# Optimization experiments

Measured on AMD Instinct MI355X. Metric: run time of the kernel, lower is better.

The kernel has to match this reference:

```python
import jax, jax.numpy as jnp
import numpy as np

M, N, NS, E, FF, OUT, L = 65536, 200000, 32, 64, 128, 128, 2

def setup_inputs() -> dict:
    key = jax.random.key(0)
    ks = jax.random.split(key, 32)
    inp = {
        'xyz': jax.random.normal(ks[0], (N, 3), jnp.float32),
        'new_xyz': jax.random.normal(ks[1], (M, 3), jnp.float32),
        'features': jax.random.normal(ks[2], (N, E), jnp.float32),
        'group_idx': jax.random.randint(ks[3], (M, NS), 0, N, jnp.int32),
        'empty_mask': jnp.zeros((M,), jnp.bool_),
        # positional MLP: Conv2d(3->E//2,1x1,no bias) + BN + ReLU + Conv2d(E//2->E,1x1)
        'pos_w1': jax.random.normal(ks[4], (E // 2, 3), jnp.float32) * 0.5,
        'pos_bn_g': jnp.ones((E // 2,), jnp.float32),
        'pos_bn_b': jnp.zeros((E // 2,), jnp.float32),
        'pos_bn_mean': jnp.zeros((E // 2,), jnp.float32),
        'pos_bn_var': jnp.ones((E // 2,), jnp.float32),
        'pos_w2': jax.random.normal(ks[5], (E, E // 2), jnp.float32) * 0.2,
        'pos_b2': jnp.zeros((E,), jnp.float32),
        # 2 pre-norm transformer layers (stacked on leading dim)
        'ln1_g': jnp.ones((L, E), jnp.float32),
        'ln1_b': jnp.zeros((L, E), jnp.float32),
        'qkv_w': jax.random.normal(ks[6], (L, 3 * E, E), jnp.float32) * (E ** -0.5),
        'qkv_b': jnp.zeros((L, 3 * E), jnp.float32),
        'attn_out_w': jax.random.normal(ks[7], (L, E, E), jnp.float32) * (E ** -0.5),
        'attn_out_b': jnp.zeros((L, E), jnp.float32),
        'ln2_g': jnp.ones((L, E), jnp.float32),
        'ln2_b': jnp.zeros((L, E), jnp.float32),
        'ff1_w': jax.random.normal(ks[8], (L, FF, E), jnp.float32) * (E ** -0.5),
        'ff1_b': jnp.zeros((L, FF), jnp.float32),
        'ff2_w': jax.random.normal(ks[9], (L, E, FF), jnp.float32) * (FF ** -0.5),
        'ff2_b': jnp.zeros((L, E), jnp.float32),
        # output Conv1d(E->OUT,1)
        'out_w': jax.random.normal(ks[10], (OUT, E), jnp.float32) * (E ** -0.5),
        'out_b': jnp.zeros((OUT,), jnp.float32),
    }
    return inp


def _layernorm(v, g, b, eps=1e-5):
    mu = v.mean(-1, keepdims=True)
    var = v.var(-1, keepdims=True)
    return (v - mu) / jnp.sqrt(var + eps) * g + b


def reference(xyz, new_xyz, features, group_idx, empty_mask,
              pos_w1, pos_bn_g, pos_bn_b, pos_bn_mean, pos_bn_var, pos_w2, pos_b2,
              ln1_g, ln1_b, qkv_w, qkv_b, attn_out_w, attn_out_b,
              ln2_g, ln2_b, ff1_w, ff1_b, ff2_w, ff2_b, out_w, out_b):
    # neighbor gather (stand-in for VoxelQueryAndGrouping)
    gf = features[group_idx]                                  # (M, NS, E)
    gx = xyz[group_idx] - new_xyz[:, None, :]                  # (M, NS, 3) relative coords
    m = empty_mask[:, None, None]
    gf = jnp.where(m, 0.0, gf)
    gx = jnp.where(m, 0.0, gx)
    # positional encoding via 1x1 convs (= per-point linear) + BN (inference stats) + ReLU
    h = gx @ pos_w1.T
    h = (h - pos_bn_mean) * pos_bn_g / jnp.sqrt(pos_bn_var + 1e-5) + pos_bn_b
    pos = jax.nn.relu(h) @ pos_w2.T + pos_b2                   # (M, NS, E)
    x = gf + pos                                               # (B=M, L=NS, E)
    d = x.shape[-1]
    scale = 1.0 / jnp.sqrt(jnp.asarray(d, x.dtype))
    n_layers = qkv_w.shape[0]
    for l in range(n_layers):
        # pre-norm self-attention (nhead=1), dropout=0
        s = _layernorm(x, ln1_g[l], ln1_b[l])
        qkv = s @ qkv_w[l].T + qkv_b[l]                        # (M, NS, 3E)
        q, k, v = jnp.split(qkv, 3, axis=-1)
        attn = jax.nn.softmax(jnp.einsum('mie,mje->mij', q * scale, k), axis=-1)
        a = jnp.einsum('mij,mje->mie', attn, v) @ attn_out_w[l].T + attn_out_b[l]
        x = x + a
        # pre-norm FFN
        s = _layernorm(x, ln2_g[l], ln2_b[l])
        f = jax.nn.relu(s @ ff1_w[l].T + ff1_b[l]) @ ff2_w[l].T + ff2_b[l]
        x = x + f
    pooled = x.max(axis=1)                                     # max over nsample window
    return pooled @ out_w.T + out_b                            # (M, OUT)
```

## Files before the change

kernel.cpp:

```cpp
#include <hip/hip_runtime.h>
#include <hip/hip_bf16.h>
#include <math.h>

#define MQ   65536
#define OUTD 128
#define ARB  18944

typedef __attribute__((ext_vector_type(8))) short bf16x8;
typedef __attribute__((ext_vector_type(4))) short bf16x4;
typedef __attribute__((ext_vector_type(4))) float f32x4;

#define WS_QKV   0
#define WS_AOW   49152
#define WS_F1W   65536
#define WS_F2W   98304
#define WS_PW2   131072
#define WS_W1F   135168
#define WS_PBF   135552

__device__ __forceinline__ unsigned short f2bf(float f) {
  unsigned u = __float_as_uint(f);
  u = (u + 0x7FFFu + ((u >> 16) & 1u)) >> 16;
  return (unsigned short)u;
}

__device__ __forceinline__ f32x4 mfma16(bf16x8 a, bf16x8 b, f32x4 c) {
  return __builtin_amdgcn_mfma_f32_16x16x32_bf16(a, b, c, 0, 0, 0);
}

__device__ __forceinline__ unsigned pk2(float a, float b) {
  union { __hip_bfloat162 h; unsigned u; } c;
  float2 p; p.x = a; p.y = b;
  c.h = __float22bfloat162_rn(p);
  return c.u;
}

__device__ __forceinline__ bf16x4 pack4(f32x4 v) {
  union { unsigned u[2]; bf16x4 s; } c;
  c.u[0] = pk2(v[0], v[1]);
  c.u[1] = pk2(v[2], v[3]);
  return c.s;
}

__device__ __forceinline__ bf16x8 pack8(const float* v) {
  union { unsigned u[4]; bf16x8 s; } c;
#pragma unroll
  for (int i = 0; i < 4; i++) c.u[i] = pk2(v[2*i], v[2*i+1]);
  return c.s;
}

__device__ __forceinline__ void cfence() { asm volatile("" ::: "memory"); }

extern "C" __global__ __launch_bounds__(256)
void convert_weights(const float* __restrict__ qkv_w, const float* __restrict__ aow,
                     const float* __restrict__ f1w,  const float* __restrict__ f2w,
                     const float* __restrict__ pw2,  const float* __restrict__ pw1,
                     const float* __restrict__ png,  const float* __restrict__ pnb,
                     const float* __restrict__ pnm,  const float* __restrict__ pnv,
                     unsigned char* __restrict__ ws) {
  int i = blockIdx.x * 256 + threadIdx.x;
  if (i < 24576) {
    ((unsigned short*)(ws + WS_QKV))[i] = f2bf(qkv_w[i]);
  } else if (i < 32768) {
    int j = i - 24576; ((unsigned short*)(ws + WS_AOW))[j] = f2bf(aow[j]);
  } else if (i < 49152) {
    int j = i - 32768; ((unsigned short*)(ws + WS_F1W))[j] = f2bf(f1w[j]);
  } else if (i < 65536) {
    int j = i - 49152; ((unsigned short*)(ws + WS_F2W))[j] = f2bf(f2w[j]);
  } else if (i < 67584) {
    int j = i - 65536; ((unsigned short*)(ws + WS_PW2))[j] = f2bf(pw2[j]);
  } else if (i < 67616) {
    int k = i - 67584;
    float s = png[k] * rsqrtf(pnv[k] + 1e-5f);
    float* w1f = (float*)(ws + WS_W1F);
    float* pbf = (float*)(ws + WS_PBF);
    w1f[k*3+0] = pw1[k*3+0] * s;
    w1f[k*3+1] = pw1[k*3+1] * s;
    w1f[k*3+2] = pw1[k*3+2] * s;
    pbf[k] = pnb[k] - pnm[k] * s;
  }
}

extern "C" __global__ __launch_bounds__(128, 2)
void nvt_mfma(const float* __restrict__ xyz,
              const float* __restrict__ new_xyz,
              const float* __restrict__ features,
              const int* __restrict__ group_idx,
              const unsigned char* __restrict__ empty_mask,
              const float* __restrict__ pos_b2,
              const float* __restrict__ ln1_g, const float* __restrict__ ln1_b,
              const float* __restrict__ qkv_b,
              const float* __restrict__ aob,
              const float* __restrict__ ln2_g, const float* __restrict__ ln2_b,
              const float* __restrict__ f1b,
              const float* __restrict__ f2b,
              const float* __restrict__ out_w, const float* __restrict__ out_b,
              const unsigned char* __restrict__ ws,
              float* __restrict__ out) {
  __shared__ __align__(16) unsigned char smem[2 * ARB];
  unsigned short *S[2], *Qb[2], *Kb[2], *Fb[2], *Vt[2], *Hs[2], *A2[2];
  float *part[2], *lnbuf[2];
#pragma unroll
  for (int G = 0; G < 2; G++) {
    unsigned char* a = smem + G * ARB;
    S[G]  = (unsigned short*)a;
    Qb[G] = (unsigned short*)(a + 4608);
    Kb[G] = (unsigned short*)(a + 9216);
    Fb[G] = (unsigned short*)(a + 4608);
    Vt[G] = (unsigned short*)(a + 13824);
    Hs[G] = S[G];
    A2[G] = Qb[G];
    part[G]  = (float*)a;
    lnbuf[G] = (float*)(a + 13824);
  }

  const unsigned short* qkvw_b = (const unsigned short*)(ws + WS_QKV);
  const unsigned short* aow_b  = (const unsigned short*)(ws + WS_AOW);
  const unsigned short* f1w_b  = (const unsigned short*)(ws + WS_F1W);
  const unsigned short* f2w_b  = (const unsigned short*)(ws + WS_F2W);
  const unsigned short* w2b    = (const unsigned short*)(ws + WS_PW2);
  const float* w1f = (const float*)(ws + WS_W1F);
  const float* pbf = (const float*)(ws + WS_PBF);

  const int tid  = threadIdx.x;
  const int w    = tid >> 6;
  const int lane = tid & 63;
  const int lr   = lane & 15;
  const int hi   = lane >> 4;
  int mg[2];
  mg[0] = blockIdx.x * 2;
  mg[1] = blockIdx.x * 2 + 1;
  bool empty[2];
  empty[0] = empty_mask[mg[0]] != 0;
  empty[1] = empty_mask[mg[1]] != 0;

#pragma unroll
  for (int G = 0; G < 2; G++) {
    int t = tid & 31, kb = tid >> 5;
    int idx = group_idx[mg[G] * 32 + t];
    float g0 = xyz[idx*3+0] - new_xyz[mg[G]*3+0];
    float g1 = xyz[idx*3+1] - new_xyz[mg[G]*3+1];
    float g2 = xyz[idx*3+2] - new_xyz[mg[G]*3+2];
    if (empty[G]) { g0 = 0.f; g1 = 0.f; g2 = 0.f; }
    float hf[8];
#pragma unroll
    for (int j = 0; j < 8; j++) {
      int k = kb * 8 + j;
      float hp = fmaf(g0, w1f[k*3+0], fmaf(g1, w1f[k*3+1], g2 * w1f[k*3+2])) + pbf[k];
      hf[j] = fmaxf(hp, 0.f);
    }
    *(bf16x8*)&Hs[G][t * 40 + kb * 8] = pack8(hf);
  }
  f32x4 x[2][2][2];
#pragma unroll
  for (int G = 0; G < 2; G++) {
    int tg0 = group_idx[mg[G] * 32 + lr];
    int tg1 = group_idx[mg[G] * 32 + 16 + lr];
#pragma unroll
    for (int mi = 0; mi < 2; mi++) {
      int mt = w + mi * 2;
      x[G][0][mi] = *(const f32x4*)(features + (size_t)tg0 * 64 + mt * 16 + hi * 4);
      x[G][1][mi] = *(const f32x4*)(features + (size_t)tg1 * 64 + mt * 16 + hi * 4);
    }
    if (empty[G]) {
#pragma unroll
      for (int nt = 0; nt < 2; nt++)
#pragma unroll
        for (int mi = 0; mi < 2; mi++) { x[G][nt][mi][0]=0.f; x[G][nt][mi][1]=0.f; x[G][nt][mi][2]=0.f; x[G][nt][mi][3]=0.f; }
    }
  }
  __syncthreads();

  {
    bf16x8 bh[2][2];
#pragma unroll
    for (int G = 0; G < 2; G++)
#pragma unroll
      for (int nt = 0; nt < 2; nt++)
        bh[G][nt] = *(const bf16x8*)&Hs[G][(nt * 16 + lr) * 40 + hi * 8];
#pragma unroll
    for (int mi = 0; mi < 2; mi++) {
      int mt = w + mi * 2;
      bf16x8 a = *(const bf16x8*)(w2b + (mt * 16 + lr) * 32 + hi * 8);
      float4 b4 = *(const float4*)(pos_b2 + mt * 16 + hi * 4);
      f32x4 bias; bias[0] = b4.x; bias[1] = b4.y; bias[2] = b4.z; bias[3] = b4.w;
#pragma unroll
      for (int G = 0; G < 2; G++)
#pragma unroll
        for (int nt = 0; nt < 2; nt++) x[G][nt][mi] += mfma16(a, bh[G][nt], bias);
    }
  }

  auto LN = [&](const float* g, const float* b) {
    float s[2][2], s2[2][2];
#pragma unroll
    for (int G = 0; G < 2; G++)
#pragma unroll
      for (int nt = 0; nt < 2; nt++) {
        float a = 0.f, a2 = 0.f;
#pragma unroll
        for (int mi = 0; mi < 2; mi++)
#pragma unroll
          for (int r = 0; r < 4; r++) { float v = x[G][nt][mi][r]; a += v; a2 = fmaf(v, v, a2); }
        a  += __shfl_xor(a, 16);  a  += __shfl_xor(a, 32);
        a2 += __shfl_xor(a2, 16); a2 += __shfl_xor(a2, 32);
        s[G][nt] = a; s2[G][nt] = a2;
      }
    if (hi == 0) {
#pragma unroll
      for (int G = 0; G < 2; G++)
#pragma unroll
        for (int nt = 0; nt < 2; nt++) {
          int tok = nt * 16 + lr;
          lnbuf[G][w * 64 + tok * 2 + 0] = s[G][nt];
          lnbuf[G][w * 64 + tok * 2 + 1] = s2[G][nt];
        }
    }
    __syncthreads();
#pragma unroll
    for (int G = 0; G < 2; G++)
#pragma unroll
      for (int nt = 0; nt < 2; nt++) {
        int tok = nt * 16 + lr;
        float st  = s[G][nt]  + lnbuf[G][(1 - w) * 64 + tok * 2 + 0];
        float s2t = s2[G][nt] + lnbuf[G][(1 - w) * 64 + tok * 2 + 1];
        float mu  = st * (1.f/64.f);
        float var = s2t * (1.f/64.f) - mu * mu;
        float inv = rsqrtf(fmaxf(var, 0.f) + 1e-5f);
#pragma unroll
        for (int mi = 0; mi < 2; mi++) {
          int mt = w + mi * 2;
          float4 g4 = *(const float4*)(g + mt * 16 + hi * 4);
          float4 b4 = *(const float4*)(b + mt * 16 + hi * 4);
          f32x4 o;
          o[0] = fmaf((x[G][nt][mi][0] - mu) * inv, g4.x, b4.x);
          o[1] = fmaf((x[G][nt][mi][1] - mu) * inv, g4.y, b4.y);
          o[2] = fmaf((x[G][nt][mi][2] - mu) * inv, g4.z, b4.z);
          o[3] = fmaf((x[G][nt][mi][3] - mu) * inv, g4.w, b4.w);
          *(bf16x4*)&S[G][tok * 72 + mt * 16 + hi * 4] = pack4(o);
        }
      }
    __syncthreads();
  };

  for (int ly = 0; ly < 2; ly++) {
    LN(ln1_g + ly*64, ln1_b + ly*64);

    {
      bf16x8 bs[2][2][2];
#pragma unroll
      for (int G = 0; G < 2; G++)
#pragma unroll
        for (int nt = 0; nt < 2; nt++)
#pragma unroll
          for (int kt = 0; kt < 2; kt++)
            bs[G][nt][kt] = *(const bf16x8*)&S[G][(nt * 16 + lr) * 72 + kt * 32 + hi * 8];
      const unsigned short* Wq = qkvw_b + ly * 192 * 64;
      const float* Bq = qkv_b + ly * 192;
#pragma unroll
      for (int mi = 0; mi < 4; mi++) {
        int mt = w + mi * 2;
        bf16x8 a0 = *(const bf16x8*)(Wq + (mt * 16 + lr) * 64 + hi * 8);
        bf16x8 a1 = *(const bf16x8*)(Wq + (mt * 16 + lr) * 64 + 32 + hi * 8);
        float4 b4 = *(const float4*)(Bq + mt * 16 + hi * 4);
#pragma unroll
        for (int G = 0; G < 2; G++)
#pragma unroll
          for (int nt = 0; nt < 2; nt++) {
            f32x4 acc; acc[0] = b4.x; acc[1] = b4.y; acc[2] = b4.z; acc[3] = b4.w;
            acc = mfma16(a0, bs[G][nt][0], acc);
            acc = mfma16(a1, bs[G][nt][1], acc);
            int t = nt * 16 + lr;
            unsigned short* dst = (mt < 4) ? Qb[G] : Kb[G];
            *(bf16x4*)&dst[t * 72 + (mt & 3) * 16 + hi * 4] = pack4(acc);
          }
      }
#pragma unroll
      for (int mvi = 0; mvi < 2; mvi++) {
        int mtv = w + mvi * 2;
        bf16x8 b0 = *(const bf16x8*)(Wq + (128 + mtv * 16 + lr) * 64 + hi * 8);
        bf16x8 b1 = *(const bf16x8*)(Wq + (128 + mtv * 16 + lr) * 64 + 32 + hi * 8);
        float bv = Bq[128 + mtv * 16 + lr];
#pragma unroll
        for (int G = 0; G < 2; G++)
#pragma unroll
          for (int nt = 0; nt < 2; nt++) {
            f32x4 acc; acc[0] = bv; acc[1] = bv; acc[2] = bv; acc[3] = bv;
            acc = mfma16(bs[G][nt][0], b0, acc);
            acc = mfma16(bs[G][nt][1], b1, acc);
            *(bf16x4*)&Vt[G][(mtv * 16 + lr) * 40 + nt * 16 + hi * 4] = pack4(acc);
          }
      }
    }
    __syncthreads();

    {
      bf16x8 ak[2][2][2], bq[2][2], av[2][4];
#pragma unroll
      for (int G = 0; G < 2; G++) {
#pragma unroll
        for (int jt = 0; jt < 2; jt++)
#pragma unroll
          for (int kt = 0; kt < 2; kt++)
            ak[G][jt][kt] = *(const bf16x8*)&Kb[G][(jt * 16 + lr) * 72 + kt * 32 + hi * 8];
#pragma unroll
        for (int kt = 0; kt < 2; kt++)
          bq[G][kt] = *(const bf16x8*)&Qb[G][(w * 16 + lr) * 72 + kt * 32 + hi * 8];
#pragma unroll
        for (int mt = 0; mt < 4; mt++)
          av[G][mt] = *(const bf16x8*)&Vt[G][(mt * 16 + lr) * 40 + hi * 8];
      }
      cfence();

#pragma unroll
      for (int G = 0; G < 2; G++) {
        f32x4 p[2];
#pragma unroll
        for (int jt = 0; jt < 2; jt++) {
          f32x4 acc; acc[0] = 0.f; acc[1] = 0.f; acc[2] = 0.f; acc[3] = 0.f;
#pragma unroll
          for (int kt = 0; kt < 2; kt++) acc = mfma16(ak[G][jt][kt], bq[G][kt], acc);
          p[jt] = acc;
        }
        float mx = -3.4e38f;
#pragma unroll
        for (int jt = 0; jt < 2; jt++)
#pragma unroll
          for (int r = 0; r < 4; r++) { p[jt][r] *= 0.125f; mx = fmaxf(mx, p[jt][r]); }
        mx = fmaxf(mx, __shfl_xor(mx, 16));
        mx = fmaxf(mx, __shfl_xor(mx, 32));
        float sum = 0.f;
#pragma unroll
        for (int jt = 0; jt < 2; jt++)
#pragma unroll
          for (int r = 0; r < 4; r++) { float e = __expf(p[jt][r] - mx); p[jt][r] = e; sum += e; }
        sum += __shfl_xor(sum, 16);
        sum += __shfl_xor(sum, 32);
        float inv = 1.f / sum;

        unsigned u[2][2];
#pragma unroll
        for (int jt = 0; jt < 2; jt++) {
          u[jt][0] = pk2(p[jt][0] * inv, p[jt][1] * inv);
          u[jt][1] = pk2(p[jt][2] * inv, p[jt][3] * inv);
        }
        int s1 = lr + 32 * (hi & 1);
        int s2 = s1 + 16;
        unsigned c0 = __shfl(u[0][0], s1), c1 = __shfl(u[0][1], s1);
        unsigned d0 = __shfl(u[0][0], s2), d1 = __shfl(u[0][1], s2);
        unsigned e0 = __shfl(u[1][0], s1), e1 = __shfl(u[1][1], s1);
        unsigned f0 = __shfl(u[1][0], s2), f1 = __shfl(u[1][1], s2);
        bool sel = (hi >> 1) != 0;
        union { unsigned uu[4]; bf16x8 v; } bp;
        bp.uu[0] = sel ? e0 : c0;
        bp.uu[1] = sel ? e1 : c1;
        bp.uu[2] = sel ? f0 : d0;
        bp.uu[3] = sel ? f1 : d1;

#pragma unroll
        for (int mt = 0; mt < 4; mt++) {
          f32x4 acc; acc[0] = 0.f; acc[1] = 0.f; acc[2] = 0.f; acc[3] = 0.f;
          acc = mfma16(av[G][mt], bp.v, acc);
          *(bf16x4*)&A2[G][(w * 16 + lr) * 72 + mt * 16 + hi * 4] = pack4(acc);
        }
      }
    }
    __syncthreads();

    {
      bf16x8 ba[2][2][2];
#pragma unroll
      for (int G = 0; G < 2; G++)
#pragma unroll
        for (int nt = 0; nt < 2; nt++)
#pragma unroll
          for (int kt = 0; kt < 2; kt++)
            ba[G][nt][kt] = *(const bf16x8*)&A2[G][(nt * 16 + lr) * 72 + kt * 32 + hi * 8];
      const unsigned short* Wo = aow_b + ly * 64 * 64;
      const float* Bo = aob + ly * 64;
#pragma unroll
      for (int mi = 0; mi < 2; mi++) {
        int mt = w + mi * 2;
        bf16x8 a0 = *(const bf16x8*)(Wo + (mt * 16 + lr) * 64 + hi * 8);
        bf16x8 a1 = *(const bf16x8*)(Wo + (mt * 16 + lr) * 64 + 32 + hi * 8);
        float4 b4 = *(const float4*)(Bo + mt * 16 + hi * 4);
#pragma unroll
        for (int G = 0; G < 2; G++)
#pragma unroll
          for (int nt = 0; nt < 2; nt++) {
            f32x4 acc; acc[0] = b4.x; acc[1] = b4.y; acc[2] = b4.z; acc[3] = b4.w;
            acc = mfma16(a0, ba[G][nt][0], acc);
            acc = mfma16(a1, ba[G][nt][1], acc);
            x[G][nt][mi] += acc;
          }
      }
    }

    LN(ln2_g + ly*64, ln2_b + ly*64);

    {
      bf16x8 bs[2][2][2];
#pragma unroll
      for (int G = 0; G < 2; G++)
#pragma unroll
        for (int nt = 0; nt < 2; nt++)
#pragma unroll
          for (int kt = 0; kt < 2; kt++)
            bs[G][nt][kt] = *(const bf16x8*)&S[G][(nt * 16 + lr) * 72 + kt * 32 + hi * 8];
      const unsigned short* W1 = f1w_b + ly * 128 * 64;
      const float* B1 = f1b + ly * 128;
#pragma unroll
      for (int mi = 0; mi < 4; mi++) {
        int mt = w + mi * 2;
        bf16x8 a0 = *(const bf16x8*)(W1 + (mt * 16 + lr) * 64 + hi * 8);
        bf16x8 a1 = *(const bf16x8*)(W1 + (mt * 16 + lr) * 64 + 32 + hi * 8);
        float4 b4 = *(const float4*)(B1 + mt * 16 + hi * 4);
#pragma unroll
        for (int G = 0; G < 2; G++)
#pragma unroll
          for (int nt = 0; nt < 2; nt++) {
            f32x4 acc; acc[0] = b4.x; acc[1] = b4.y; acc[2] = b4.z; acc[3] = b4.w;
            acc = mfma16(a0, bs[G][nt][0], acc);
            acc = mfma16(a1, bs[G][nt][1], acc);
#pragma unroll
            for (int r = 0; r < 4; r++) acc[r] = fmaxf(acc[r], 0.f);
            *(bf16x4*)&Fb[G][(nt * 16 + lr) * 136 + mt * 16 + hi * 4] = pack4(acc);
          }
      }
    }
    __syncthreads();

    {
      bf16x8 bfr[2][2][4];
#pragma unroll
      for (int G = 0; G < 2; G++)
#pragma unroll
        for (int nt = 0; nt < 2; nt++)
#pragma unroll
          for (int kt = 0; kt < 4; kt++)
            bfr[G][nt][kt] = *(const bf16x8*)&Fb[G][(nt * 16 + lr) * 136 + kt * 32 + hi * 8];
      const unsigned short* W2 = f2w_b + ly * 64 * 128;
      const float* B2 = f2b + ly * 64;
#pragma unroll
      for (int mi = 0; mi < 2; mi++) {
        int mt = w + mi * 2;
        bf16x8 a[4];
#pragma unroll
        for (int kt = 0; kt < 4; kt++)
          a[kt] = *(const bf16x8*)(W2 + (mt * 16 + lr) * 128 + kt * 32 + hi * 8);
        float4 b4 = *(const float4*)(B2 + mt * 16 + hi * 4);
#pragma unroll
        for (int G = 0; G < 2; G++)
#pragma unroll
          for (int nt = 0; nt < 2; nt++) {
            f32x4 acc; acc[0] = b4.x; acc[1] = b4.y; acc[2] = b4.z; acc[3] = b4.w;
#pragma unroll
            for (int kt = 0; kt < 4; kt++) acc = mfma16(a[kt], bfr[G][nt][kt], acc);
            x[G][nt][mi] += acc;
          }
      }
    }
  }

#pragma unroll
  for (int G = 0; G < 2; G++) {
    f32x4 pm[2];
#pragma unroll
    for (int mi = 0; mi < 2; mi++)
#pragma unroll
      for (int r = 0; r < 4; r++) pm[mi][r] = fmaxf(x[G][0][mi][r], x[G][1][mi][r]);
#pragma unroll
    for (int d = 1; d < 16; d <<= 1)
#pragma unroll
      for (int mi = 0; mi < 2; mi++)
#pragma unroll
        for (int r = 0; r < 4; r++) pm[mi][r] = fmaxf(pm[mi][r], __shfl_xor(pm[mi][r], d));
    if (lr == 0) {
#pragma unroll
      for (int mi = 0; mi < 2; mi++) {
        int mt = w + mi * 2;
        *(f32x4*)&part[G][mt * 16 + hi * 4] = pm[mi];
      }
    }
  }
  __syncthreads();

  {
    int o = tid;
    const float* wr = out_w + o * 64;
    float a0[2] = {0.f, 0.f}, a1[2] = {0.f, 0.f}, a2[2] = {0.f, 0.f}, a3[2] = {0.f, 0.f};
#pragma unroll
    for (int i = 0; i < 16; i++) {
      float4 wv = *(const float4*)(wr + i * 4);
#pragma unroll
      for (int G = 0; G < 2; G++) {
        float4 pv = *(const float4*)&part[G][i * 4];
        a0[G] = fmaf(pv.x, wv.x, a0[G]);
        a1[G] = fmaf(pv.y, wv.y, a1[G]);
        a2[G] = fmaf(pv.z, wv.z, a2[G]);
        a3[G] = fmaf(pv.w, wv.w, a3[G]);
      }
    }
    float ob = out_b[o];
#pragma unroll
    for (int G = 0; G < 2; G++)
      out[(size_t)mg[G] * OUTD + o] = ob + (a0[G] + a1[G]) + (a2[G] + a3[G]);
  }
}

extern "C" void kernel_launch(void* const* d_in, const int* in_sizes, int n_in,
                              void* d_out, int out_size, void* d_ws, size_t ws_size,
                              hipStream_t stream) {
  const float* xyz         = (const float*)d_in[0];
  const float* new_xyz     = (const float*)d_in[1];
  const float* features    = (const float*)d_in[2];
  const int*   group_idx   = (const int*)d_in[3];
  const unsigned char* empty_mask = (const unsigned char*)d_in[4];
  const float* pos_w1      = (const float*)d_in[5];
  const float* pos_bn_g    = (const float*)d_in[6];
  const float* pos_bn_b    = (const float*)d_in[7];
  const float* pos_bn_mean = (const float*)d_in[8];
  const float* pos_bn_var  = (const float*)d_in[9];
  const float* pos_w2      = (const float*)d_in[10];
  const float* pos_b2      = (const float*)d_in[11];
  const float* ln1_g       = (const float*)d_in[12];
  const float* ln1_b       = (const float*)d_in[13];
  const float* qkv_w       = (const float*)d_in[14];
  const float* qkv_b       = (const float*)d_in[15];
  const float* aow         = (const float*)d_in[16];
  const float* aob         = (const float*)d_in[17];
  const float* ln2_g       = (const float*)d_in[18];
  const float* ln2_b       = (const float*)d_in[19];
  const float* f1w         = (const float*)d_in[20];
  const float* f1b         = (const float*)d_in[21];
  const float* f2w         = (const float*)d_in[22];
  const float* f2b         = (const float*)d_in[23];
  const float* out_w       = (const float*)d_in[24];
  const float* out_b       = (const float*)d_in[25];
  float* out = (float*)d_out;
  unsigned char* ws = (unsigned char*)d_ws;

  hipLaunchKernelGGL(convert_weights, dim3(265), dim3(256), 0, stream,
                     qkv_w, aow, f1w, f2w, pos_w2, pos_w1,
                     pos_bn_g, pos_bn_b, pos_bn_mean, pos_bn_var, ws);

  hipLaunchKernelGGL(nvt_mfma, dim3(MQ / 2), dim3(128), 0, stream,
                     xyz, new_xyz, features, group_idx, empty_mask,
                     pos_b2, ln1_g, ln1_b, qkv_b, aob, ln2_g, ln2_b,
                     f1b, f2b, out_w, out_b, ws, out);
}
```

Before: 943.3 us.

## Split each block's work across four waves instead of two

Doubles the block to 256 threads. Each wave now owns one 16-column slice of the embedding instead of two, and the attention stage maps one wave per (group, query tile) pair instead of looping over both groups. This cuts per-thread register state and the serial MFMA chain per wave, aiming for more waves in flight and better latency hiding. In exchange, the LayerNorm cross-wave reduction now reads four partial sums, and barriers span more waves.

Measured after the change: 1.211 ms. 28.3% more time.

```diff
diff --git a/kernel.cpp b/kernel.cpp
--- a/kernel.cpp
+++ b/kernel.cpp
@@ -81,7 +81,7 @@
   }
 }
 
-extern "C" __global__ __launch_bounds__(128, 2)
+extern "C" __global__ __launch_bounds__(256, 3)
 void nvt_mfma(const float* __restrict__ xyz,
               const float* __restrict__ new_xyz,
               const float* __restrict__ features,
@@ -136,7 +136,7 @@
 
 #pragma unroll
   for (int G = 0; G < 2; G++) {
-    int t = tid & 31, kb = tid >> 5;
+    int t = tid & 31, kb = (tid >> 5) & 3;
     int idx = group_idx[mg[G] * 32 + t];
     float g0 = xyz[idx*3+0] - new_xyz[mg[G]*3+0];
     float g1 = xyz[idx*3+1] - new_xyz[mg[G]*3+1];
@@ -151,22 +151,16 @@
     }
     *(bf16x8*)&Hs[G][t * 40 + kb * 8] = pack8(hf);
   }
-  f32x4 x[2][2][2];
+  f32x4 x[2][2];
 #pragma unroll
   for (int G = 0; G < 2; G++) {
     int tg0 = group_idx[mg[G] * 32 + lr];
     int tg1 = group_idx[mg[G] * 32 + 16 + lr];
-#pragma unroll
-    for (int mi = 0; mi < 2; mi++) {
-      int mt = w + mi * 2;
-      x[G][0][mi] = *(const f32x4*)(features + (size_t)tg0 * 64 + mt * 16 + hi * 4);
-      x[G][1][mi] = *(const f32x4*)(features + (size_t)tg1 * 64 + mt * 16 + hi * 4);
-    }
+    x[G][0] = *(const f32x4*)(features + (size_t)tg0 * 64 + w * 16 + hi * 4);
+    x[G][1] = *(const f32x4*)(features + (size_t)tg1 * 64 + w * 16 + hi * 4);
     if (empty[G]) {
 #pragma unroll
-      for (int nt = 0; nt < 2; nt++)
-#pragma unroll
-        for (int mi = 0; mi < 2; mi++) { x[G][nt][mi][0]=0.f; x[G][nt][mi][1]=0.f; x[G][nt][mi][2]=0.f; x[G][nt][mi][3]=0.f; }
+      for (int nt = 0; nt < 2; nt++) { x[G][nt][0]=0.f; x[G][nt][1]=0.f; x[G][nt][2]=0.f; x[G][nt][3]=0.f; }
     }
   }
   __syncthreads();
@@ -178,17 +172,13 @@
 #pragma unroll
       for (int nt = 0; nt < 2; nt++)
         bh[G][nt] = *(const bf16x8*)&Hs[G][(nt * 16 + lr) * 40 + hi * 8];
-#pragma unroll
-    for (int mi = 0; mi < 2; mi++) {
-      int mt = w + mi * 2;
-      bf16x8 a = *(const bf16x8*)(w2b + (mt * 16 + lr) * 32 + hi * 8);
-      float4 b4 = *(const float4*)(pos_b2 + mt * 16 + hi * 4);
-      f32x4 bias; bias[0] = b4.x; bias[1] = b4.y; bias[2] = b4.z; bias[3] = b4.w;
-#pragma unroll
-      for (int G = 0; G < 2; G++)
-#pragma unroll
-        for (int nt = 0; nt < 2; nt++) x[G][nt][mi] += mfma16(a, bh[G][nt], bias);
-    }
+    bf16x8 a = *(const bf16x8*)(w2b + (w * 16 + lr) * 32 + hi * 8);
+    float4 b4 = *(const float4*)(pos_b2 + w * 16 + hi * 4);
+    f32x4 bias; bias[0] = b4.x; bias[1] = b4.y; bias[2] = b4.z; bias[3] = b4.w;
+#pragma unroll
+    for (int G = 0; G < 2; G++)
+#pragma unroll
+      for (int nt = 0; nt < 2; nt++) x[G][nt] += mfma16(a, bh[G][nt], bias);
   }
 
   auto LN = [&](const float* g, const float* b) {
@@ -199,9 +189,7 @@
       for (int nt = 0; nt < 2; nt++) {
         float a = 0.f, a2 = 0.f;
 #pragma unroll
-        for (int mi = 0; mi < 2; mi++)
-#pragma unroll
-          for (int r = 0; r < 4; r++) { float v = x[G][nt][mi][r]; a += v; a2 = fmaf(v, v, a2); }
+        for (int r = 0; r < 4; r++) { float v = x[G][nt][r]; a += v; a2 = fmaf(v, v, a2); }
         a  += __shfl_xor(a, 16);  a  += __shfl_xor(a, 32);
         a2 += __shfl_xor(a2, 16); a2 += __shfl_xor(a2, 32);
         s[G][nt] = a; s2[G][nt] = a2;
@@ -222,23 +210,23 @@
 #pragma unroll
       for (int nt = 0; nt < 2; nt++) {
         int tok = nt * 16 + lr;
-        float st  = s[G][nt]  + lnbuf[G][(1 - w) * 64 + tok * 2 + 0];
-        float s2t = s2[G][nt] + lnbuf[G][(1 - w) * 64 + tok * 2 + 1];
+        float st = 0.f, s2t = 0.f;
+#pragma unroll
+        for (int w2_ = 0; w2_ < 4; w2_++) {
+          st  += lnbuf[G][w2_ * 64 + tok * 2 + 0];
+          s2t += lnbuf[G][w2_ * 64 + tok * 2 + 1];
+        }
         float mu  = st * (1.f/64.f);
         float var = s2t * (1.f/64.f) - mu * mu;
         float inv = rsqrtf(fmaxf(var, 0.f) + 1e-5f);
-#pragma unroll
-        for (int mi = 0; mi < 2; mi++) {
-          int mt = w + mi * 2;
-          float4 g4 = *(const float4*)(g + mt * 16 + hi * 4);
-          float4 b4 = *(const float4*)(b + mt * 16 + hi * 4);
-          f32x4 o;
-          o[0] = fmaf((x[G][nt][mi][0] - mu) * inv, g4.x, b4.x);
-          o[1] = fmaf((x[G][nt][mi][1] - mu) * inv, g4.y, b4.y);
-          o[2] = fmaf((x[G][nt][mi][2] - mu) * inv, g4.z, b4.z);
-          o[3] = fmaf((x[G][nt][mi][3] - mu) * inv, g4.w, b4.w);
-          *(bf16x4*)&S[G][tok * 72 + mt * 16 + hi * 4] = pack4(o);
-        }
+        float4 g4 = *(const float4*)(g + w * 16 + hi * 4);
+        float4 b4 = *(const float4*)(b + w * 16 + hi * 4);
+        f32x4 o;
+        o[0] = fmaf((x[G][nt][0] - mu) * inv, g4.x, b4.x);
+        o[1] = fmaf((x[G][nt][1] - mu) * inv, g4.y, b4.y);
+        o[2] = fmaf((x[G][nt][2] - mu) * inv, g4.z, b4.z);
+        o[3] = fmaf((x[G][nt][3] - mu) * inv, g4.w, b4.w);
+        *(bf16x4*)&S[G][tok * 72 + w * 16 + hi * 4] = pack4(o);
       }
     __syncthreads();
   };
@@ -258,8 +246,8 @@
       const unsigned short* Wq = qkvw_b + ly * 192 * 64;
       const float* Bq = qkv_b + ly * 192;
 #pragma unroll
-      for (int mi = 0; mi < 4; mi++) {
-        int mt = w + mi * 2;
+      for (int mi = 0; mi < 2; mi++) {
+        int mt = w + mi * 4;
         bf16x8 a0 = *(const bf16x8*)(Wq + (mt * 16 + lr) * 64 + hi * 8);
         bf16x8 a1 = *(const bf16x8*)(Wq + (mt * 16 + lr) * 64 + 32 + hi * 8);
         float4 b4 = *(const float4*)(Bq + mt * 16 + hi * 4);
@@ -275,12 +263,10 @@
             *(bf16x4*)&dst[t * 72 + (mt & 3) * 16 + hi * 4] = pack4(acc);
           }
       }
-#pragma unroll
-      for (int mvi = 0; mvi < 2; mvi++) {
-        int mtv = w + mvi * 2;
-        bf16x8 b0 = *(const bf16x8*)(Wq + (128 + mtv * 16 + lr) * 64 + hi * 8);
-        bf16x8 b1 = *(const bf16x8*)(Wq + (128 + mtv * 16 + lr) * 64 + 32 + hi * 8);
-        float bv = Bq[128 + mtv * 16 + lr];
+      {
+        bf16x8 b0 = *(const bf16x8*)(Wq + (128 + w * 16 + lr) * 64 + hi * 8);
+        bf16x8 b1 = *(const bf16x8*)(Wq + (128 + w * 16 + lr) * 64 + 32 + hi * 8);
+        float bv = Bq[128 + w * 16 + lr];
 #pragma unroll
         for (int G = 0; G < 2; G++)
 #pragma unroll
@@ -288,81 +274,81 @@
             f32x4 acc; acc[0] = bv; acc[1] = bv; acc[2] = bv; acc[3] = bv;
             acc = mfma16(bs[G][nt][0], b0, acc);
             acc = mfma16(bs[G][nt][1], b1, acc);
-            *(bf16x4*)&Vt[G][(mtv * 16 + lr) * 40 + nt * 16 + hi * 4] = pack4(acc);
+            *(bf16x4*)&Vt[G][(w * 16 + lr) * 40 + nt * 16 + hi * 4] = pack4(acc);
           }
       }
     }
     __syncthreads();
 
     {
-      bf16x8 ak[2][2][2], bq[2][2], av[2][4];
-#pragma unroll
-      for (int G = 0; G < 2; G++) {
-#pragma unroll
-        for (int jt = 0; jt < 2; jt++)
-#pragma unroll
-          for (int kt = 0; kt < 2; kt++)
-            ak[G][jt][kt] = *(const bf16x8*)&Kb[G][(jt * 16 + lr) * 72 + kt * 32 + hi * 8];
+      const int Gm = w >> 1;
+      const int it = w & 1;
+      unsigned short* Kg = (unsigned short*)(smem + Gm * ARB + 9216);
+      unsigned short* Qg = (unsigned short*)(smem + Gm * ARB + 4608);
+      unsigned short* Vg = (unsigned short*)(smem + Gm * ARB + 13824);
+      unsigned short* Ag = Qg;
+      bf16x8 ak[2][2], bq[2], av[4];
+#pragma unroll
+      for (int jt = 0; jt < 2; jt++)
 #pragma unroll
         for (int kt = 0; kt < 2; kt++)
-          bq[G][kt] = *(const bf16x8*)&Qb[G][(w * 16 + lr) * 72 + kt * 32 + hi * 8];
-#pragma unroll
-        for (int mt = 0; mt < 4; mt++)
-          av[G][mt] = *(const bf16x8*)&Vt[G][(mt * 16 + lr) * 40 + hi * 8];
-      }
+          ak[jt][kt] = *(const bf16x8*)&Kg[(jt * 16 + lr) * 72 + kt * 32 + hi * 8];
+#pragma unroll
+      for (int kt = 0; kt < 2; kt++)
+        bq[kt] = *(const bf16x8*)&Qg[(it * 16 + lr) * 72 + kt * 32 + hi * 8];
+#pragma unroll
+      for (int mt = 0; mt < 4; mt++)
+        av[mt] = *(const bf16x8*)&Vg[(mt * 16 + lr) * 40 + hi * 8];
       cfence();
 
-#pragma unroll
-      for (int G = 0; G < 2; G++) {
-        f32x4 p[2];
-#pragma unroll
-        for (int jt = 0; jt < 2; jt++) {
-          f32x4 acc; acc[0] = 0.f; acc[1] = 0.f; acc[2] = 0.f; acc[3] = 0.f;
-#pragma unroll
-          for (int kt = 0; kt < 2; kt++) acc = mfma16(ak[G][jt][kt], bq[G][kt], acc);
-          p[jt] = acc;
-        }
-        float mx = -3.4e38f;
-#pragma unroll
-        for (int jt = 0; jt < 2; jt++)
-#pragma unroll
-          for (int r = 0; r < 4; r++) { p[jt][r] *= 0.125f; mx = fmaxf(mx, p[jt][r]); }
-        mx = fmaxf(mx, __shfl_xor(mx, 16));
-        mx = fmaxf(mx, __shfl_xor(mx, 32));
-        float sum = 0.f;
-#pragma unroll
-        for (int jt = 0; jt < 2; jt++)
-#pragma unroll
-          for (int r = 0; r < 4; r++) { float e = __expf(p[jt][r] - mx); p[jt][r] = e; sum += e; }
-        sum += __shfl_xor(sum, 16);
-        sum += __shfl_xor(sum, 32);
-        float inv = 1.f / sum;
-
-        unsigned u[2][2];
-#pragma unroll
-        for (int jt = 0; jt < 2; jt++) {
-          u[jt][0] = pk2(p[jt][0] * inv, p[jt][1] * inv);
-          u[jt][1] = pk2(p[jt][2] * inv, p[jt][3] * inv);
-        }
-        int s1 = lr + 32 * (hi & 1);
-        int s2 = s1 + 16;
-        unsigned c0 = __shfl(u[0][0], s1), c1 = __shfl(u[0][1], s1);
-        unsigned d0 = __shfl(u[0][0], s2), d1 = __shfl(u[0][1], s2);
-        unsigned e0 = __shfl(u[1][0], s1), e1 = __shfl(u[1][1], s1);
-        unsigned f0 = __shfl(u[1][0], s2), f1 = __shfl(u[1][1], s2);
-        bool sel = (hi >> 1) != 0;
-        union { unsigned uu[4]; bf16x8 v; } bp;
-        bp.uu[0] = sel ? e0 : c0;
-        bp.uu[1] = sel ? e1 : c1;
-        bp.uu[2] = sel ? f0 : d0;
-        bp.uu[3] = sel ? f1 : d1;
-
-#pragma unroll
-        for (int mt = 0; mt < 4; mt++) {
-          f32x4 acc; acc[0] = 0.f; acc[1] = 0.f; acc[2] = 0.f; acc[3] = 0.f;
-          acc = mfma16(av[G][mt], bp.v, acc);
-          *(bf16x4*)&A2[G][(w * 16 + lr) * 72 + mt * 16 + hi * 4] = pack4(acc);
-        }
+      f32x4 p[2];
+#pragma unroll
+      for (int jt = 0; jt < 2; jt++) {
+        f32x4 acc; acc[0] = 0.f; acc[1] = 0.f; acc[2] = 0.f; acc[3] = 0.f;
+#pragma unroll
+        for (int kt = 0; kt < 2; kt++) acc = mfma16(ak[jt][kt], bq[kt], acc);
+        p[jt] = acc;
+      }
+      float mx = -3.4e38f;
+#pragma unroll
+      for (int jt = 0; jt < 2; jt++)
+#pragma unroll
+        for (int r = 0; r < 4; r++) { p[jt][r] *= 0.125f; mx = fmaxf(mx, p[jt][r]); }
+      mx = fmaxf(mx, __shfl_xor(mx, 16));
+      mx = fmaxf(mx, __shfl_xor(mx, 32));
+      float sum = 0.f;
+#pragma unroll
+      for (int jt = 0; jt < 2; jt++)
+#pragma unroll
+        for (int r = 0; r < 4; r++) { float e = __expf(p[jt][r] - mx); p[jt][r] = e; sum += e; }
+      sum += __shfl_xor(sum, 16);
+      sum += __shfl_xor(sum, 32);
+      float inv = 1.f / sum;
+
+      unsigned u[2][2];
+#pragma unroll
+      for (int jt = 0; jt < 2; jt++) {
+        u[jt][0] = pk2(p[jt][0] * inv, p[jt][1] * inv);
+        u[jt][1] = pk2(p[jt][2] * inv, p[jt][3] * inv);
+      }
+      int s1 = lr + 32 * (hi & 1);
+      int s2 = s1 + 16;
+      unsigned c0 = __shfl(u[0][0], s1), c1 = __shfl(u[0][1], s1);
+      unsigned d0 = __shfl(u[0][0], s2), d1 = __shfl(u[0][1], s2);
+      unsigned e0 = __shfl(u[1][0], s1), e1 = __shfl(u[1][1], s1);
+      unsigned f0 = __shfl(u[1][0], s2), f1 = __shfl(u[1][1], s2);
+      bool sel = (hi >> 1) != 0;
+      union { unsigned uu[4]; bf16x8 v; } bp;
+      bp.uu[0] = sel ? e0 : c0;
+      bp.uu[1] = sel ? e1 : c1;
+      bp.uu[2] = sel ? f0 : d0;
+      bp.uu[3] = sel ? f1 : d1;
+
+#pragma unroll
+      for (int mt = 0; mt < 4; mt++) {
+        f32x4 acc; acc[0] = 0.f; acc[1] = 0.f; acc[2] = 0.f; acc[3] = 0.f;
+        acc = mfma16(av[mt], bp.v, acc);
+        *(bf16x4*)&Ag[(it * 16 + lr) * 72 + mt * 16 + hi * 4] = pack4(acc);
       }
     }
     __syncthreads();
@@ -378,22 +364,18 @@
             ba[G][nt][kt] = *(const bf16x8*)&A2[G][(nt * 16 + lr) * 72 + kt * 32 + hi * 8];
       const unsigned short* Wo = aow_b + ly * 64 * 64;
       const float* Bo = aob + ly * 64;
-#pragma unroll
-      for (int mi = 0; mi < 2; mi++) {
-        int mt = w + mi * 2;
-        bf16x8 a0 = *(const bf16x8*)(Wo + (mt * 16 + lr) * 64 + hi * 8);
-        bf16x8 a1 = *(const bf16x8*)(Wo + (mt * 16 + lr) * 64 + 32 + hi * 8);
-        float4 b4 = *(const float4*)(Bo + mt * 16 + hi * 4);
-#pragma unroll
-        for (int G = 0; G < 2; G++)
-#pragma unroll
-          for (int nt = 0; nt < 2; nt++) {
-            f32x4 acc; acc[0] = b4.x; acc[1] = b4.y; acc[2] = b4.z; acc[3] = b4.w;
-            acc = mfma16(a0, ba[G][nt][0], acc);
-            acc = mfma16(a1, ba[G][nt][1], acc);
-            x[G][nt][mi] += acc;
-          }
-      }
+      bf16x8 a0 = *(const bf16x8*)(Wo + (w * 16 + lr) * 64 + hi * 8);
+      bf16x8 a1 = *(const bf16x8*)(Wo + (w * 16 + lr) * 64 + 32 + hi * 8);
+      float4 b4 = *(const float4*)(Bo + w * 16 + hi * 4);
+#pragma unroll
+      for (int G = 0; G < 2; G++)
+#pragma unroll
+        for (int nt = 0; nt < 2; nt++) {
+          f32x4 acc; acc[0] = b4.x; acc[1] = b4.y; acc[2] = b4.z; acc[3] = b4.w;
+          acc = mfma16(a0, ba[G][nt][0], acc);
+          acc = mfma16(a1, ba[G][nt][1], acc);
+          x[G][nt] += acc;
+        }
     }
 
     LN(ln2_g + ly*64, ln2_b + ly*64);
@@ -410,8 +392,8 @@
       const unsigned short* W1 = f1w_b + ly * 128 * 64;
       const float* B1 = f1b + ly * 128;
 #pragma unroll
-      for (int mi = 0; mi < 4; mi++) {
-        int mt = w + mi * 2;
+      for (int mi = 0; mi < 2; mi++) {
+        int mt = w + mi * 4;
         bf16x8 a0 = *(const bf16x8*)(W1 + (mt * 16 + lr) * 64 + hi * 8);
         bf16x8 a1 = *(const bf16x8*)(W1 + (mt * 16 + lr) * 64 + 32 + hi * 8);
         float4 b4 = *(const float4*)(B1 + mt * 16 + hi * 4);
@@ -441,70 +423,50 @@
             bfr[G][nt][kt] = *(const bf16x8*)&Fb[G][(nt * 16 + lr) * 136 + kt * 32 + hi * 8];
       const unsigned short* W2 = f2w_b + ly * 64 * 128;
       const float* B2 = f2b + ly * 64;
-#pragma unroll
-      for (int mi = 0; mi < 2; mi++) {
-        int mt = w + mi * 2;
-        bf16x8 a[4];
-#pragma unroll
-        for (int kt = 0; kt < 4; kt++)
-          a[kt] = *(const bf16x8*)(W2 + (mt * 16 + lr) * 128 + kt * 32 + hi * 8);
-        float4 b4 = *(const float4*)(B2 + mt * 16 + hi * 4);
-#pragma unroll
-        for (int G = 0; G < 2; G++)
-#pragma unroll
-          for (int nt = 0; nt < 2; nt++) {
-            f32x4 acc; acc[0] = b4.x; acc[1] = b4.y; acc[2] = b4.z; acc[3] = b4.w;
-#pragma unroll
-            for (int kt = 0; kt < 4; kt++) acc = mfma16(a[kt], bfr[G][nt][kt], acc);
-            x[G][nt][mi] += acc;
-          }
-      }
+      bf16x8 a[4];
+#pragma unroll
+      for (int kt = 0; kt < 4; kt++)
+        a[kt] = *(const bf16x8*)(W2 + (w * 16 + lr) * 128 + kt * 32 + hi * 8);
+      float4 b4 = *(const float4*)(B2 + w * 16 + hi * 4);
+#pragma unroll
+      for (int G = 0; G < 2; G++)
+#pragma unroll
+        for (int nt = 0; nt < 2; nt++) {
+          f32x4 acc; acc[0] = b4.x; acc[1] = b4.y; acc[2] = b4.z; acc[3] = b4.w;
+#pragma unroll
+          for (int kt = 0; kt < 4; kt++) acc = mfma16(a[kt], bfr[G][nt][kt], acc);
+          x[G][nt] += acc;
+        }
     }
   }
 
 #pragma unroll
   for (int G = 0; G < 2; G++) {
-    f32x4 pm[2];
-#pragma unroll
-    for (int mi = 0; mi < 2; mi++)
-#pragma unroll
-      for (int r = 0; r < 4; r++) pm[mi][r] = fmaxf(x[G][0][mi][r], x[G][1][mi][r]);
+    f32x4 pm;
+#pragma unroll
+    for (int r = 0; r < 4; r++) pm[r] = fmaxf(x[G][0][r], x[G][1][r]);
 #pragma unroll
     for (int d = 1; d < 16; d <<= 1)
 #pragma unroll
-      for (int mi = 0; mi < 2; mi++)
-#pragma unroll
-        for (int r = 0; r < 4; r++) pm[mi][r] = fmaxf(pm[mi][r], __shfl_xor(pm[mi][r], d));
-    if (lr == 0) {
-#pragma unroll
-      for (int mi = 0; mi < 2; mi++) {
-        int mt = w + mi * 2;
-        *(f32x4*)&part[G][mt * 16 + hi * 4] = pm[mi];
-      }
-    }
+      for (int r = 0; r < 4; r++) pm[r] = fmaxf(pm[r], __shfl_xor(pm[r], d));
+    if (lr == 0) *(f32x4*)&part[G][w * 16 + hi * 4] = pm;
   }
   __syncthreads();
 
   {
-    int o = tid;
+    int o = tid & 127, G = tid >> 7;
     const float* wr = out_w + o * 64;
-    float a0[2] = {0.f, 0.f}, a1[2] = {0.f, 0.f}, a2[2] = {0.f, 0.f}, a3[2] = {0.f, 0.f};
+    float a0 = 0.f, a1 = 0.f, a2 = 0.f, a3 = 0.f;
 #pragma unroll
     for (int i = 0; i < 16; i++) {
       float4 wv = *(const float4*)(wr + i * 4);
-#pragma unroll
-      for (int G = 0; G < 2; G++) {
-        float4 pv = *(const float4*)&part[G][i * 4];
-        a0[G] = fmaf(pv.x, wv.x, a0[G]);
-        a1[G] = fmaf(pv.y, wv.y, a1[G]);
-        a2[G] = fmaf(pv.z, wv.z, a2[G]);
-        a3[G] = fmaf(pv.w, wv.w, a3[G]);
-      }
-    }
-    float ob = out_b[o];
-#pragma unroll
-    for (int G = 0; G < 2; G++)
-      out[(size_t)mg[G] * OUTD + o] = ob + (a0[G] + a1[G]) + (a2[G] + a3[G]);
+      float4 pv = *(const float4*)&part[G][i * 4];
+      a0 = fmaf(pv.x, wv.x, a0);
+      a1 = fmaf(pv.y, wv.y, a1);
+      a2 = fmaf(pv.z, wv.z, a2);
+      a3 = fmaf(pv.w, wv.w, a3);
+    }
+    out[(size_t)mg[G] * OUTD + o] = out_b[o] + (a0 + a1) + (a2 + a3);
   }
 }
 
@@ -544,7 +506,7 @@
                      qkv_w, aow, f1w, f2w, pos_w2, pos_w1,
                      pos_bn_g, pos_bn_b, pos_bn_mean, pos_bn_var, ws);
 
-  hipLaunchKernelGGL(nvt_mfma, dim3(MQ / 2), dim3(128), 0, stream,
+  hipLaunchKernelGGL(nvt_mfma, dim3(MQ / 2), dim3(256), 0, stream,
                      xyz, new_xyz, features, group_idx, empty_mask,
                      pos_b2, ln1_g, ln1_b, qkv_b, aob, ln2_g, ln2_b,
                      f1b, f2b, out_w, out_b, ws, out);
```
